# Kernel optimization log

Hardware: AMD Instinct MI355X
Metric: run time of the kernel (lower is better)

The kernel has to match this reference:

```python
import jax, jax.numpy as jnp
import numpy as np

D_KEY = 128
INF = 1e9  # stands in for the module's global INF constant


def setup_inputs() -> dict:
    key = jax.random.key(0)
    kq, kk, kv = jax.random.split(key, 3)
    B, S, D = 8, 4096, D_KEY
    return {
        "query": jax.random.normal(kq, (B, S, D), dtype=jnp.float32),
        "keys": jax.random.normal(kk, (B, S, D), dtype=jnp.float32),
        "values": jax.random.normal(kv, (B, S, D), dtype=jnp.float32),
    }


def reference(query, keys, values):
    # dot_products: [B, Sq, Sk]
    scores = jnp.einsum("bqd,bkd->bqk", query, keys)
    S = scores.shape[-1]
    # causal: subtract INF on strict upper triangle (triu(1)), applied BEFORE scaling
    causal = jnp.triu(jnp.ones((S, S), dtype=scores.dtype), 1) * INF
    logits = (scores - causal[None, :, :]) / jnp.asarray(np.sqrt(D_KEY), scores.dtype)
    # legacy F.softmax on 3D transposed tensor == softmax over key axis
    probs = jax.nn.softmax(logits, axis=-1)
    # dropout with p=0.0 is identity
    return jnp.einsum("bqk,bkd->bqd", probs, values)
```

## Files before the change

kernel.cpp:

```cpp
#include <hip/hip_runtime.h>

#define B_SZ   8
#define S_LEN  4096
#define D_K    128
#define KB     64
#define CH     8
#define NCHUNK 1152
#define NC(q)  (((q) + 4) >> 2)

typedef short  short8  __attribute__((ext_vector_type(8)));
typedef float  floatx4 __attribute__((ext_vector_type(4)));

#if defined(__has_builtin)
#if __has_builtin(__builtin_amdgcn_exp2f)
#define EXP2F(x) __builtin_amdgcn_exp2f(x)
#endif
#endif
#ifndef EXP2F
#define EXP2F(x) exp2f(x)
#endif

__device__ __forceinline__ unsigned bfround(float x) {
  unsigned u = __builtin_bit_cast(unsigned, x);
  return (u + 0x7fffu + ((u >> 16) & 1u)) >> 16;
}
__device__ __forceinline__ unsigned bfpack2(float a, float b) {
  return bfround(a) | (bfround(b) << 16);
}
__device__ __forceinline__ unsigned cvtpk(float lo, float hi) {
  unsigned r;
  asm("v_cvt_pk_bf16_f32 %0, %1, %2" : "=v"(r) : "v"(lo), "v"(hi));
  return r;
}


__device__ __forceinline__ void dma16(const void* g, const void* l) {
  __builtin_amdgcn_global_load_lds(
      (__attribute__((address_space(1))) unsigned int*)(unsigned long long)g,
      (__attribute__((address_space(3))) unsigned int*)(unsigned int)(unsigned long long)l,
      16, 0, 0);
}


__global__ __launch_bounds__(256)
void prep(const float* __restrict__ K, const float* __restrict__ V,
          unsigned short* __restrict__ Kb, unsigned short* __restrict__ Vt,
          int* __restrict__ cnt) {
  __shared__ float tile[64][129];
  const int tid = threadIdx.x;
  const int bid = blockIdx.x;
  if (bid == 0 && tid == 0) *cnt = 0;
  const int b   = bid >> 6;
  const int s   = bid & 63;
  const int kt  = s * 64;

  {
    const int r  = tid >> 2;
    const int cq = tid & 3;
    const float* kp = K + (size_t)(b * S_LEN + kt + r) * D_K + cq * 32;
    unsigned short* kdst = Kb + (size_t)bid * 8192 + r * 128;
    const int xr = (r & 7) << 4;
#pragma unroll
    for (int jj = 0; jj < 4; ++jj) {
      float4 f0 = *(const float4*)(kp + jj * 8);
      float4 f1 = *(const float4*)(kp + jj * 8 + 4);
      uint4 u;
      u.x = bfpack2(f0.x, f0.y);
      u.y = bfpack2(f0.z, f0.w);
      u.z = bfpack2(f1.x, f1.y);
      u.w = bfpack2(f1.z, f1.w);
      const int o = (cq * 64 + jj * 16) ^ xr;
      *(uint4*)(kdst + (o >> 1)) = u;
    }
  }

  {
    const int k  = tid >> 2;
    const int cq = tid & 3;
    const float* vp = V + (size_t)(b * S_LEN + kt + k) * D_K + cq * 32;
#pragma unroll
    for (int i = 0; i < 8; ++i) {
      float4 f = *(const float4*)(vp + i * 4);
      tile[k][cq * 32 + i * 4]     = f.x;
      tile[k][cq * 32 + i * 4 + 1] = f.y;
      tile[k][cq * 32 + i * 4 + 2] = f.z;
      tile[k][cq * 32 + i * 4 + 3] = f.w;
    }
  }
  __syncthreads();

  {
    const int d = tid >> 1;
    const int h = tid & 1;
    unsigned short* vdst = Vt + (size_t)bid * 8192 + d * 64;
    const int xr = (d & 7) << 4;
#pragma unroll
    for (int jj = 0; jj < 4; ++jj) {
      const int k0 = h * 32 + jj * 8;
      uint4 u;
      u.x = bfpack2(tile[k0 + 0][d], tile[k0 + 1][d]);
      u.y = bfpack2(tile[k0 + 2][d], tile[k0 + 3][d]);
      u.z = bfpack2(tile[k0 + 4][d], tile[k0 + 5][d]);
      u.w = bfpack2(tile[k0 + 6][d], tile[k0 + 7][d]);
      const int o = (h * 64 + jj * 16) ^ xr;
      *(uint4*)(vdst + (o >> 1)) = u;
    }
  }
}


__global__ __launch_bounds__(256, 2)
void attn_worker(const float* __restrict__ Q, const unsigned short* __restrict__ Kb,
                 const unsigned short* __restrict__ Vt, int* __restrict__ cnt,
                 float* __restrict__ ml, float* __restrict__ pO) {
  __shared__ __align__(16) short Klds[2][8192];
  __shared__ __align__(16) short Vtlds[8192];
  __shared__ int s_chunk;

  const int tid  = threadIdx.x;
  const int lane = tid & 63;
  const int w    = tid >> 6;
  const int l15  = lane & 15;
  const int quad = lane >> 4;
  const int xk   = (l15 & 7) << 3;

  const float CSC = 0.12752041f;

  for (;;) {
    if (tid == 0) s_chunk = atomicAdd(cnt, 1);
    __syncthreads();
    const int c = s_chunk;
    if (c >= NCHUNK) break;

    const int b = c & 7;
    int q = 31, r = c >> 3;
    while (r >= NC(q)) { r -= NC(q); --q; }
    const int j  = r;
    const int q0 = q * 128;
    const int s0 = j * CH;
    const int s1 = min(s0 + CH, 2 * q + 2);

    short8 bq[2][4];
    int qg[2];
#pragma unroll
    for (int sub = 0; sub < 2; ++sub) {
      qg[sub] = q0 + w * 32 + sub * 16 + l15;
      const float* qrow = Q + (size_t)(b * S_LEN + qg[sub]) * D_K + quad * 8;
#pragma unroll
      for (int kd = 0; kd < 4; ++kd) {
        float4 f0 = *(const float4*)(qrow + kd * 32);
        float4 f1 = *(const float4*)(qrow + kd * 32 + 4);
        union { short8 s; unsigned u[4]; } tt;
        tt.u[0] = bfpack2(f0.x, f0.y);
        tt.u[1] = bfpack2(f0.z, f0.w);
        tt.u[2] = bfpack2(f1.x, f1.y);
        tt.u[3] = bfpack2(f1.z, f1.w);
        bq[sub][kd] = tt.s;
      }
    }

    floatx4 acc[2][8];
#pragma unroll
    for (int sub = 0; sub < 2; ++sub)
#pragma unroll
      for (int nc = 0; nc < 8; ++nc) acc[sub][nc] = (floatx4){0.f, 0.f, 0.f, 0.f};
    float m_run[2] = {-1e30f, -1e30f}, l_run[2] = {0.f, 0.f};

    const unsigned short* kb0 = Kb + (size_t)b * 64 * 8192;
    const unsigned short* vb0 = Vt + (size_t)b * 64 * 8192;
    const int lo = lane * 8;

#define STAGE_K(BUF, S)                                                        \
    do {                                                                       \
      const unsigned short* kg_ = kb0 + (size_t)(S) * 8192 + w * 2048 + lo;    \
      short* kl_ = &Klds[BUF][w * 2048];                                       \
      _Pragma("unroll")                                                        \
      for (int i_ = 0; i_ < 4; ++i_) dma16(kg_ + i_ * 512, kl_ + i_ * 512);    \
    } while (0)
#define STAGE_V(S)                                                             \
    do {                                                                       \
      const unsigned short* vg_ = vb0 + (size_t)(S) * 8192 + w * 2048 + lo;    \
      short* vl_ = &Vtlds[w * 2048];                                           \
      _Pragma("unroll")                                                        \
      for (int i_ = 0; i_ < 4; ++i_) dma16(vg_ + i_ * 512, vl_ + i_ * 512);    \
    } while (0)

    STAGE_K(s0 & 1, s0);
    if (s0 + 1 < s1) STAGE_K((s0 + 1) & 1, s0 + 1);
    STAGE_V(s0);
    asm volatile("s_waitcnt vmcnt(0)" ::: "memory");
    __builtin_amdgcn_s_barrier();
    __builtin_amdgcn_sched_barrier(0);

    for (int s = s0; s < s1; ++s) {
      const int kt  = s * KB;
      const int cur = s & 1;
      const short* Kl = &Klds[cur][0];
      const bool act = (kt <= q0 + w * 32 + 31);

      floatx4 st[2][4];
      if (act) {
        __builtin_amdgcn_s_setprio(1);
#pragma unroll
        for (int kf = 0; kf < 4; ++kf) {
          floatx4 c0 = (floatx4){0.f, 0.f, 0.f, 0.f};
          floatx4 c1 = (floatx4){0.f, 0.f, 0.f, 0.f};
#pragma unroll
          for (int kd = 0; kd < 4; ++kd) {
            short8 a = *(const short8*)(&Kl[((kf * 16 + l15) << 7) + ((kd * 32 + quad * 8) ^ xk)]);
            c0 = __builtin_amdgcn_mfma_f32_16x16x32_bf16(a, bq[0][kd], c0, 0, 0, 0);
            c1 = __builtin_amdgcn_mfma_f32_16x16x32_bf16(a, bq[1][kd], c1, 0, 0, 0);
          }
          st[0][kf] = c0;
          st[1][kf] = c1;
        }
        __builtin_amdgcn_s_setprio(0);

#pragma unroll
        for (int sub = 0; sub < 2; ++sub) {
          if (kt + 63 > q0 + w * 32 + sub * 16) {
#pragma unroll
            for (int kf = 0; kf < 4; ++kf)
#pragma unroll
              for (int rr = 0; rr < 4; ++rr) {
                int key = kt + kf * 16 + quad * 4 + rr;
                if (key > qg[sub]) st[sub][kf][rr] = -1e30f;
              }
          }
        }
      }

      asm volatile("s_waitcnt vmcnt(0)" ::: "memory");
      __builtin_amdgcn_s_barrier();
      __builtin_amdgcn_sched_barrier(0);

      short8 pa[2][2];
      if (act) {
        short* pw = &Klds[cur][(w * 16 + l15) << 6];
#pragma unroll
        for (int sub = 0; sub < 2; ++sub) {
          float mx = st[sub][0][0];
#pragma unroll
          for (int kf = 0; kf < 4; ++kf)
#pragma unroll
            for (int rr = 0; rr < 4; ++rr) mx = fmaxf(mx, st[sub][kf][rr]);
          mx = fmaxf(mx, __shfl_xor(mx, 16, 64));
          mx = fmaxf(mx, __shfl_xor(mx, 32, 64));
          const float m_new = fmaxf(m_run[sub], mx);
          const bool  grow  = __any(m_new > m_run[sub]);

          float p[4][4];
          float tsum = 0.f;
#pragma unroll
          for (int kf = 0; kf < 4; ++kf)
#pragma unroll
            for (int rr = 0; rr < 4; ++rr) {
              p[kf][rr] = EXP2F((st[sub][kf][rr] - m_new) * CSC);
              tsum += p[kf][rr];
            }
          tsum += __shfl_xor(tsum, 16, 64);
          tsum += __shfl_xor(tsum, 32, 64);

          if (grow) {
            const float alpha = EXP2F((m_run[sub] - m_new) * CSC);
            l_run[sub] = l_run[sub] * alpha + tsum;
#pragma unroll
            for (int rr = 0; rr < 4; ++rr) {
              const float ar = __shfl(alpha, quad * 4 + rr, 64);
#pragma unroll
              for (int nc = 0; nc < 8; ++nc) acc[sub][nc][rr] *= ar;
            }
          } else {
            l_run[sub] = l_run[sub] + tsum;
          }
          m_run[sub] = m_new;

#pragma unroll
          for (int kf = 0; kf < 4; ++kf) {
            uint2 u;
            u.x = cvtpk(p[kf][0], p[kf][1]);
            u.y = cvtpk(p[kf][2], p[kf][3]);
            *(uint2*)(&pw[(kf * 16 + quad * 4) ^ xk]) = u;
          }
          __asm__ __volatile__("" ::: "memory");
          pa[sub][0] = *(const short8*)(&pw[(quad * 8) ^ xk]);
          pa[sub][1] = *(const short8*)(&pw[(32 + quad * 8) ^ xk]);
          __asm__ __volatile__("" ::: "memory");
        }

        __builtin_amdgcn_s_setprio(1);
#pragma unroll
        for (int nc = 0; nc < 8; ++nc) {
          short8 bv0 = *(const short8*)(&Vtlds[((nc * 16 + l15) << 6) + ((quad * 8) ^ xk)]);
          short8 bv1 = *(const short8*)(&Vtlds[((nc * 16 + l15) << 6) + ((32 + quad * 8) ^ xk)]);
          acc[0][nc] = __builtin_amdgcn_mfma_f32_16x16x32_bf16(pa[0][0], bv0, acc[0][nc], 0, 0, 0);
          acc[0][nc] = __builtin_amdgcn_mfma_f32_16x16x32_bf16(pa[0][1], bv1, acc[0][nc], 0, 0, 0);
          acc[1][nc] = __builtin_amdgcn_mfma_f32_16x16x32_bf16(pa[1][0], bv0, acc[1][nc], 0, 0, 0);
          acc[1][nc] = __builtin_amdgcn_mfma_f32_16x16x32_bf16(pa[1][1], bv1, acc[1][nc], 0, 0, 0);
        }
        __builtin_amdgcn_s_setprio(0);
      }

      asm volatile("s_waitcnt lgkmcnt(0)" ::: "memory");
      __builtin_amdgcn_s_barrier();
      __builtin_amdgcn_sched_barrier(0);
      if (s + 2 < s1) STAGE_K(cur, s + 2);
      if (s + 1 < s1) STAGE_V(s + 1);
    }
#undef STAGE_K
#undef STAGE_V

    float* po = pO + (size_t)c * 16384;
#pragma unroll
    for (int sub = 0; sub < 2; ++sub) {
#pragma unroll
      for (int rr = 0; rr < 4; ++rr) {
        const int qrow = w * 32 + sub * 16 + quad * 4 + rr;
        float* op = po + qrow * D_K + l15;
#pragma unroll
        for (int nc = 0; nc < 8; ++nc) op[nc * 16] = acc[sub][nc][rr];
      }
      if (quad == 0) {
        const int qrow = w * 32 + sub * 16 + l15;
        ml[(size_t)c * 256 + qrow * 2]     = m_run[sub];
        ml[(size_t)c * 256 + qrow * 2 + 1] = l_run[sub];
      }
    }
  }
}


__global__ __launch_bounds__(256)
void attn_combine(const float* __restrict__ ml, const float* __restrict__ pO,
                  float* __restrict__ O) {
  const int t = blockIdx.x;
  const int b = t >> 5;
  const int q = t & 31;
  const float CSC = 0.12752041f;

  const int tid = threadIdx.x;
  const int ql  = tid >> 1;
  const int dh  = (tid & 1) * 64;

  int cum = 0;
  for (int tq = 31; tq > q; --tq) cum += NC(tq);
  const int ncb = NC(q);

  float m[8], l[8], wgt[8];
  float M = -1e30f;
#pragma unroll
  for (int i = 0; i < 8; ++i) {
    if (i < ncb) {
      const size_t slot = (size_t)((cum + i) << 3 | b);
      m[i] = ml[slot * 256 + ql * 2];
      l[i] = ml[slot * 256 + ql * 2 + 1];
      M = fmaxf(M, m[i]);
    }
  }
  float L = 0.f;
#pragma unroll
  for (int i = 0; i < 8; ++i)
    if (i < ncb) { wgt[i] = EXP2F((m[i] - M) * CSC); L += wgt[i] * l[i]; }
  const float inv = 1.0f / L;

  float4 out[16];
#pragma unroll
  for (int v = 0; v < 16; ++v) out[v] = make_float4(0.f, 0.f, 0.f, 0.f);
#pragma unroll
  for (int i = 0; i < 8; ++i) {
    if (i < ncb) {
      const size_t slot = (size_t)((cum + i) << 3 | b);
      const float* src = pO + slot * 16384 + ql * D_K + dh;
      const float wj = wgt[i];
#pragma unroll
      for (int v = 0; v < 16; ++v) {
        float4 f = *(const float4*)(src + v * 4);
        out[v].x += wj * f.x;  out[v].y += wj * f.y;
        out[v].z += wj * f.z;  out[v].w += wj * f.w;
      }
    }
  }
  float* dst = O + ((size_t)(b * S_LEN) + q * 128 + ql) * D_K + dh;
#pragma unroll
  for (int v = 0; v < 16; ++v) {
    *(float4*)(dst + v * 4) = make_float4(out[v].x * inv, out[v].y * inv,
                                          out[v].z * inv, out[v].w * inv);
  }
}


#define KT_STR 136
#define VT_STR 72
#define PT_STR 72

__global__ __launch_bounds__(256, 2)
void attn_fwd_fb(const float* __restrict__ Q, const float* __restrict__ K,
                 const float* __restrict__ V, float* __restrict__ O) {
  __shared__ __align__(16) short Klds[KB * KT_STR];
  __shared__ __align__(16) short Vtlds[D_K * VT_STR];
  __shared__ __align__(16) short Plds[4 * 16 * PT_STR];

  const int tid  = threadIdx.x;
  const int lane = tid & 63;
  const int w    = tid >> 6;
  const int l15  = lane & 15;
  const int quad = lane >> 4;

  const int bid = blockIdx.x;
  const int b   = bid & 7;
  const int qi  = 63 - (bid >> 3);
  const int q0  = qi * 64;

  const float CSC = 0.12752041f;

  const int    qg   = q0 + w * 16 + l15;
  const float* qrow = Q + (size_t)(b * S_LEN + qg) * D_K + quad * 8;
  short8 bq[4];
#pragma unroll
  for (int kd = 0; kd < 4; ++kd) {
    float4 f0 = *(const float4*)(qrow + kd * 32);
    float4 f1 = *(const float4*)(qrow + kd * 32 + 4);
    union { short8 s; unsigned u[4]; } t;
    t.u[0] = bfpack2(f0.x, f0.y);
    t.u[1] = bfpack2(f0.z, f0.w);
    t.u[2] = bfpack2(f1.x, f1.y);
    t.u[3] = bfpack2(f1.z, f1.w);
    bq[kd] = t.s;
  }

  floatx4 acc[8];
#pragma unroll
  for (int nc = 0; nc < 8; ++nc) acc[nc] = (floatx4){0.f, 0.f, 0.f, 0.f};
  float m_run = -1e30f, l_run = 0.f;

  const int d4 = tid & 31;
  const int kq = tid >> 5;
  const int nsteps = qi + 1;

  for (int s = 0; s < nsteps; ++s) {
    const int kt = s * KB;
#pragma unroll
    for (int r2 = 0; r2 < 2; ++r2) {
      const int row = r2 * 32 + kq * 4;
      const float* kp = K + (size_t)(b * S_LEN + kt + row) * D_K + d4 * 4;
      const float* vp = V + (size_t)(b * S_LEN + kt + row) * D_K + d4 * 4;
      float4 fk[4], fv[4];
#pragma unroll
      for (int i = 0; i < 4; ++i) {
        fk[i] = *(const float4*)(kp + i * D_K);
        fv[i] = *(const float4*)(vp + i * D_K);
      }
#pragma unroll
      for (int i = 0; i < 4; ++i) {
        uint2 u;
        u.x = bfpack2(fk[i].x, fk[i].y);
        u.y = bfpack2(fk[i].z, fk[i].w);
        *(uint2*)(&Klds[(row + i) * KT_STR + d4 * 4]) = u;
      }
#pragma unroll
      for (int c = 0; c < 4; ++c) {
        float e0 = ((const float*)&fv[0])[c];
        float e1 = ((const float*)&fv[1])[c];
        float e2 = ((const float*)&fv[2])[c];
        float e3 = ((const float*)&fv[3])[c];
        uint2 u;
        u.x = bfpack2(e0, e1);
        u.y = bfpack2(e2, e3);
        *(uint2*)(&Vtlds[(d4 * 4 + c) * VT_STR + row]) = u;
      }
    }
    __syncthreads();

    floatx4 st[4];
#pragma unroll
    for (int kf = 0; kf < 4; ++kf) {
      floatx4 cc = (floatx4){0.f, 0.f, 0.f, 0.f};
#pragma unroll
      for (int kd = 0; kd < 4; ++kd) {
        short8 a = *(const short8*)(&Klds[(kf * 16 + l15) * KT_STR + kd * 32 + quad * 8]);
        cc = __builtin_amdgcn_mfma_f32_16x16x32_bf16(a, bq[kd], cc, 0, 0, 0);
      }
      st[kf] = cc;
    }

    if (s == nsteps - 1) {
#pragma unroll
      for (int kf = 0; kf < 4; ++kf)
#pragma unroll
        for (int rr = 0; rr < 4; ++rr) {
          int key = kt + kf * 16 + quad * 4 + rr;
          if (key > qg) st[kf][rr] = -1e30f;
        }
    }

    float mx = st[0][0];
#pragma unroll
    for (int kf = 0; kf < 4; ++kf)
#pragma unroll
      for (int rr = 0; rr < 4; ++rr) mx = fmaxf(mx, st[kf][rr]);
    mx = fmaxf(mx, __shfl_xor(mx, 16, 64));
    mx = fmaxf(mx, __shfl_xor(mx, 32, 64));
    const float m_new = fmaxf(m_run, mx);
    const float alpha = EXP2F((m_run - m_new) * CSC);

    float p[4][4];
    float tsum = 0.f;
#pragma unroll
    for (int kf = 0; kf < 4; ++kf)
#pragma unroll
      for (int rr = 0; rr < 4; ++rr) {
        p[kf][rr] = EXP2F((st[kf][rr] - m_new) * CSC);
        tsum += p[kf][rr];
      }
    tsum += __shfl_xor(tsum, 16, 64);
    tsum += __shfl_xor(tsum, 32, 64);
    l_run = l_run * alpha + tsum;
    m_run = m_new;

#pragma unroll
    for (int rr = 0; rr < 4; ++rr) {
      const float ar = __shfl(alpha, quad * 4 + rr, 64);
#pragma unroll
      for (int nc = 0; nc < 8; ++nc) acc[nc][rr] *= ar;
    }

    short* pw = &Plds[(w * 16 + l15) * PT_STR];
#pragma unroll
    for (int kf = 0; kf < 4; ++kf) {
      uint2 u;
      u.x = bfpack2(p[kf][0], p[kf][1]);
      u.y = bfpack2(p[kf][2], p[kf][3]);
      *(uint2*)(&pw[kf * 16 + quad * 4]) = u;
    }
    __asm__ __volatile__("" ::: "memory");
    short8 pa0 = *(const short8*)(&pw[quad * 8]);
    short8 pa1 = *(const short8*)(&pw[32 + quad * 8]);

#pragma unroll
    for (int nc = 0; nc < 8; ++nc) {
      short8 bv0 = *(const short8*)(&Vtlds[(nc * 16 + l15) * VT_STR + quad * 8]);
      acc[nc] = __builtin_amdgcn_mfma_f32_16x16x32_bf16(pa0, bv0, acc[nc], 0, 0, 0);
      short8 bv1 = *(const short8*)(&Vtlds[(nc * 16 + l15) * VT_STR + 32 + quad * 8]);
      acc[nc] = __builtin_amdgcn_mfma_f32_16x16x32_bf16(pa1, bv1, acc[nc], 0, 0, 0);
    }
    __syncthreads();
  }

#pragma unroll
  for (int rr = 0; rr < 4; ++rr) {
    const float lr  = __shfl(l_run, quad * 4 + rr, 64);
    const float inv = 1.0f / lr;
    const int qout  = q0 + w * 16 + quad * 4 + rr;
    float* op = O + (size_t)(b * S_LEN + qout) * D_K + l15;
#pragma unroll
    for (int nc = 0; nc < 8; ++nc) op[nc * 16] = acc[nc][rr] * inv;
  }
}


extern "C" void kernel_launch(void* const* d_in, const int* in_sizes, int n_in,
                              void* d_out, int out_size, void* d_ws, size_t ws_size,
                              hipStream_t stream) {
  const float* Q = (const float*)d_in[0];
  const float* K = (const float*)d_in[1];
  const float* V = (const float*)d_in[2];
  float* O = (float*)d_out;

  const size_t elems = (size_t)B_SZ * S_LEN * D_K;

  const size_t off_ml = 256;
  const size_t off_po = off_ml + (size_t)NCHUNK * 256 * 4;
  const size_t off_kb = off_po + (size_t)NCHUNK * 16384 * 4;
  const size_t off_vt = off_kb + elems * 2;
  const size_t need   = off_vt + elems * 2;

  if (ws_size >= need) {
    char* ws = (char*)d_ws;
    int*            cnt = (int*)ws;
    float*          mlp = (float*)(ws + off_ml);
    float*          po  = (float*)(ws + off_po);
    unsigned short* Kbp = (unsigned short*)(ws + off_kb);
    unsigned short* Vtp = (unsigned short*)(ws + off_vt);

    prep<<<dim3(B_SZ * 64), dim3(256), 0, stream>>>(K, V, Kbp, Vtp, cnt);
    attn_worker<<<dim3(768), dim3(256), 0, stream>>>(Q, Kbp, Vtp, cnt, mlp, po);
    attn_combine<<<dim3(256), dim3(256), 0, stream>>>(mlp, po, O);
  } else {
    attn_fwd_fb<<<dim3(512), dim3(256), 0, stream>>>(Q, K, V, O);
  }
}
```

Before: 188.6 us.

## Store partial attention outputs in bf16 and interleave the two softmax sub-tiles

The worker now writes its per-chunk partial output accumulators as bf16 instead of fp32. This halves the workspace written by the worker and read back by the combine kernel, which now unpacks short8 loads. The online softmax handles both 16-row sub-tiles side by side for more instruction-level parallelism. It also keeps the row-sum per lane and reduces it across lanes only once at the end, dropping two shuffles per key tile. The cost is extra rounding error in the partial outputs before they are merged.

```diff
diff --git a/kernel.cpp b/kernel.cpp
--- a/kernel.cpp
+++ b/kernel.cpp
@@ -26,6 +26,9 @@
 }
 __device__ __forceinline__ unsigned bfpack2(float a, float b) {
   return bfround(a) | (bfround(b) << 16);
+}
+__device__ __forceinline__ float bf2f(unsigned short s) {
+  return __builtin_bit_cast(float, ((unsigned)s) << 16);
 }
 __device__ __forceinline__ unsigned cvtpk(float lo, float hi) {
   unsigned r;
@@ -112,7 +115,7 @@
 __global__ __launch_bounds__(256, 2)
 void attn_worker(const float* __restrict__ Q, const unsigned short* __restrict__ Kb,
                  const unsigned short* __restrict__ Vt, int* __restrict__ cnt,
-                 float* __restrict__ ml, float* __restrict__ pO) {
+                 float* __restrict__ ml, unsigned short* __restrict__ pO) {
   __shared__ __align__(16) short Klds[2][8192];
   __shared__ __align__(16) short Vtlds[8192];
   __shared__ int s_chunk;
@@ -236,57 +239,73 @@
 
       short8 pa[2][2];
       if (act) {
-        short* pw = &Klds[cur][(w * 16 + l15) << 6];
-#pragma unroll
-        for (int sub = 0; sub < 2; ++sub) {
-          float mx = st[sub][0][0];
-#pragma unroll
-          for (int kf = 0; kf < 4; ++kf)
-#pragma unroll
-            for (int rr = 0; rr < 4; ++rr) mx = fmaxf(mx, st[sub][kf][rr]);
-          mx = fmaxf(mx, __shfl_xor(mx, 16, 64));
-          mx = fmaxf(mx, __shfl_xor(mx, 32, 64));
-          const float m_new = fmaxf(m_run[sub], mx);
-          const bool  grow  = __any(m_new > m_run[sub]);
-
-          float p[4][4];
-          float tsum = 0.f;
-#pragma unroll
-          for (int kf = 0; kf < 4; ++kf)
-#pragma unroll
-            for (int rr = 0; rr < 4; ++rr) {
-              p[kf][rr] = EXP2F((st[sub][kf][rr] - m_new) * CSC);
-              tsum += p[kf][rr];
-            }
-          tsum += __shfl_xor(tsum, 16, 64);
-          tsum += __shfl_xor(tsum, 32, 64);
-
-          if (grow) {
-            const float alpha = EXP2F((m_run[sub] - m_new) * CSC);
-            l_run[sub] = l_run[sub] * alpha + tsum;
-#pragma unroll
-            for (int rr = 0; rr < 4; ++rr) {
-              const float ar = __shfl(alpha, quad * 4 + rr, 64);
-#pragma unroll
-              for (int nc = 0; nc < 8; ++nc) acc[sub][nc][rr] *= ar;
-            }
-          } else {
-            l_run[sub] = l_run[sub] + tsum;
+        float mx0 = st[0][0][0], mx1 = st[1][0][0];
+#pragma unroll
+        for (int kf = 0; kf < 4; ++kf)
+#pragma unroll
+          for (int rr = 0; rr < 4; ++rr) {
+            mx0 = fmaxf(mx0, st[0][kf][rr]);
+            mx1 = fmaxf(mx1, st[1][kf][rr]);
           }
-          m_run[sub] = m_new;
-
-#pragma unroll
-          for (int kf = 0; kf < 4; ++kf) {
-            uint2 u;
-            u.x = cvtpk(p[kf][0], p[kf][1]);
-            u.y = cvtpk(p[kf][2], p[kf][3]);
-            *(uint2*)(&pw[(kf * 16 + quad * 4) ^ xk]) = u;
+        mx0 = fmaxf(mx0, __shfl_xor(mx0, 16, 64));
+        mx1 = fmaxf(mx1, __shfl_xor(mx1, 16, 64));
+        mx0 = fmaxf(mx0, __shfl_xor(mx0, 32, 64));
+        mx1 = fmaxf(mx1, __shfl_xor(mx1, 32, 64));
+        const float mn0 = fmaxf(m_run[0], mx0);
+        const float mn1 = fmaxf(m_run[1], mx1);
+        const bool  g0  = __any(mn0 > m_run[0]);
+        const bool  g1  = __any(mn1 > m_run[1]);
+
+        float t0 = 0.f, t1 = 0.f;
+#pragma unroll
+        for (int kf = 0; kf < 4; ++kf)
+#pragma unroll
+          for (int rr = 0; rr < 4; ++rr) {
+            st[0][kf][rr] = EXP2F((st[0][kf][rr] - mn0) * CSC); t0 += st[0][kf][rr];
+            st[1][kf][rr] = EXP2F((st[1][kf][rr] - mn1) * CSC); t1 += st[1][kf][rr];
           }
-          __asm__ __volatile__("" ::: "memory");
-          pa[sub][0] = *(const short8*)(&pw[(quad * 8) ^ xk]);
-          pa[sub][1] = *(const short8*)(&pw[(32 + quad * 8) ^ xk]);
-          __asm__ __volatile__("" ::: "memory");
+
+        if (g0) {
+          const float a0 = EXP2F((m_run[0] - mn0) * CSC);
+          l_run[0] = l_run[0] * a0 + t0;
+#pragma unroll
+          for (int rr = 0; rr < 4; ++rr) {
+            const float ar = __shfl(a0, quad * 4 + rr, 64);
+#pragma unroll
+            for (int nc = 0; nc < 8; ++nc) acc[0][nc][rr] *= ar;
+          }
+        } else l_run[0] += t0;
+        if (g1) {
+          const float a1 = EXP2F((m_run[1] - mn1) * CSC);
+          l_run[1] = l_run[1] * a1 + t1;
+#pragma unroll
+          for (int rr = 0; rr < 4; ++rr) {
+            const float ar = __shfl(a1, quad * 4 + rr, 64);
+#pragma unroll
+            for (int nc = 0; nc < 8; ++nc) acc[1][nc][rr] *= ar;
+          }
+        } else l_run[1] += t1;
+        m_run[0] = mn0;
+        m_run[1] = mn1;
+
+        short* pw0 = &Klds[cur][(w * 16 + l15) << 6];
+        short* pw1 = pw0 + 4096;
+#pragma unroll
+        for (int kf = 0; kf < 4; ++kf) {
+          uint2 u0, u1;
+          u0.x = cvtpk(st[0][kf][0], st[0][kf][1]);
+          u0.y = cvtpk(st[0][kf][2], st[0][kf][3]);
+          u1.x = cvtpk(st[1][kf][0], st[1][kf][1]);
+          u1.y = cvtpk(st[1][kf][2], st[1][kf][3]);
+          *(uint2*)(&pw0[(kf * 16 + quad * 4) ^ xk]) = u0;
+          *(uint2*)(&pw1[(kf * 16 + quad * 4) ^ xk]) = u1;
         }
+        __asm__ __volatile__("" ::: "memory");
+        pa[0][0] = *(const short8*)(&pw0[(quad * 8) ^ xk]);
+        pa[0][1] = *(const short8*)(&pw0[(32 + quad * 8) ^ xk]);
+        pa[1][0] = *(const short8*)(&pw1[(quad * 8) ^ xk]);
+        pa[1][1] = *(const short8*)(&pw1[(32 + quad * 8) ^ xk]);
+        __asm__ __volatile__("" ::: "memory");
 
         __builtin_amdgcn_s_setprio(1);
 #pragma unroll
@@ -310,20 +329,23 @@
 #undef STAGE_K
 #undef STAGE_V
 
-    float* po = pO + (size_t)c * 16384;
+    unsigned short* po = pO + (size_t)c * 16384;
 #pragma unroll
     for (int sub = 0; sub < 2; ++sub) {
+      float lf = l_run[sub];
+      lf += __shfl_xor(lf, 16, 64);
+      lf += __shfl_xor(lf, 32, 64);
 #pragma unroll
       for (int rr = 0; rr < 4; ++rr) {
         const int qrow = w * 32 + sub * 16 + quad * 4 + rr;
-        float* op = po + qrow * D_K + l15;
-#pragma unroll
-        for (int nc = 0; nc < 8; ++nc) op[nc * 16] = acc[sub][nc][rr];
+        unsigned short* op = po + qrow * D_K + l15;
+#pragma unroll
+        for (int nc = 0; nc < 8; ++nc) op[nc * 16] = (unsigned short)bfround(acc[sub][nc][rr]);
       }
       if (quad == 0) {
         const int qrow = w * 32 + sub * 16 + l15;
         ml[(size_t)c * 256 + qrow * 2]     = m_run[sub];
-        ml[(size_t)c * 256 + qrow * 2 + 1] = l_run[sub];
+        ml[(size_t)c * 256 + qrow * 2 + 1] = lf;
       }
     }
   }
@@ -331,7 +353,7 @@
 
 
 __global__ __launch_bounds__(256)
-void attn_combine(const float* __restrict__ ml, const float* __restrict__ pO,
+void attn_combine(const float* __restrict__ ml, const unsigned short* __restrict__ pO,
                   float* __restrict__ O) {
   const int t = blockIdx.x;
   const int b = t >> 5;
@@ -363,28 +385,29 @@
     if (i < ncb) { wgt[i] = EXP2F((m[i] - M) * CSC); L += wgt[i] * l[i]; }
   const float inv = 1.0f / L;
 
-  float4 out[16];
-#pragma unroll
-  for (int v = 0; v < 16; ++v) out[v] = make_float4(0.f, 0.f, 0.f, 0.f);
+  float out[64];
+#pragma unroll
+  for (int v = 0; v < 64; ++v) out[v] = 0.f;
 #pragma unroll
   for (int i = 0; i < 8; ++i) {
     if (i < ncb) {
       const size_t slot = (size_t)((cum + i) << 3 | b);
-      const float* src = pO + slot * 16384 + ql * D_K + dh;
+      const unsigned short* src = pO + slot * 16384 + ql * D_K + dh;
       const float wj = wgt[i];
 #pragma unroll
-      for (int v = 0; v < 16; ++v) {
-        float4 f = *(const float4*)(src + v * 4);
-        out[v].x += wj * f.x;  out[v].y += wj * f.y;
-        out[v].z += wj * f.z;  out[v].w += wj * f.w;
+      for (int v = 0; v < 8; ++v) {
+        short8 s8 = *(const short8*)(src + v * 8);
+#pragma unroll
+        for (int e = 0; e < 8; ++e)
+          out[v * 8 + e] += wj * bf2f((unsigned short)s8[e]);
       }
     }
   }
   float* dst = O + ((size_t)(b * S_LEN) + q * 128 + ql) * D_K + dh;
 #pragma unroll
   for (int v = 0; v < 16; ++v) {
-    *(float4*)(dst + v * 4) = make_float4(out[v].x * inv, out[v].y * inv,
-                                          out[v].z * inv, out[v].w * inv);
+    *(float4*)(dst + v * 4) = make_float4(out[v * 4] * inv, out[v * 4 + 1] * inv,
+                                          out[v * 4 + 2] * inv, out[v * 4 + 3] * inv);
   }
 }
 
@@ -570,7 +593,7 @@
 
   const size_t off_ml = 256;
   const size_t off_po = off_ml + (size_t)NCHUNK * 256 * 4;
-  const size_t off_kb = off_po + (size_t)NCHUNK * 16384 * 4;
+  const size_t off_kb = off_po + (size_t)NCHUNK * 32768;
   const size_t off_vt = off_kb + elems * 2;
   const size_t need   = off_vt + elems * 2;
 
@@ -578,7 +601,7 @@
     char* ws = (char*)d_ws;
     int*            cnt = (int*)ws;
     float*          mlp = (float*)(ws + off_ml);
-    float*          po  = (float*)(ws + off_po);
+    unsigned short* po  = (unsigned short*)(ws + off_po);
     unsigned short* Kbp = (unsigned short*)(ws + off_kb);
     unsigned short* Vtp = (unsigned short*)(ws + off_vt);
 
```

After: 184.1 us. 2.4% less time.
